# Optimization experiments

Measured on AMD Instinct MI355X. Metric: run time of the kernel, lower is better.

## Reference

```python
import jax, jax.numpy as jnp
import numpy as np

B, L, D = 32, 2048, 64
MASK_FILL = -1.0e6  # matches torch code's -1000000.0


def setup_inputs() -> dict:
    key = jax.random.key(0)
    kq, kk, kv, kl = jax.random.split(key, 4)
    queries = jax.random.normal(kq, (B, L, D), dtype=jnp.float32)
    keys = jax.random.normal(kk, (B, L, D), dtype=jnp.float32)
    values = jax.random.normal(kv, (B, L, D), dtype=jnp.float32)
    valid_lens = jax.random.randint(kl, (B,), 1, L + 1, dtype=jnp.int64)
    return {"queries": queries, "keys": keys, "values": values,
            "valid_lens": valid_lens}


def reference(queries, keys, values, valid_lens):
    d = queries.shape[-1]
    # [B, Lq, Lk] scores
    scores = jnp.einsum('bqd,bkd->bqk', queries, keys) / jnp.sqrt(
        jnp.asarray(d, dtype=queries.dtype))
    # length mask: position k valid iff k < valid_lens[b]
    Lk = scores.shape[-1]
    mask = jnp.arange(Lk)[None, :] < valid_lens[:, None]      # [B, Lk]
    scores = jnp.where(mask[:, None, :], scores, MASK_FILL)   # broadcast over Lq
    attn = jax.nn.softmax(scores, axis=-1)
    # dropout p=0.0 -> identity
    return jnp.einsum('bqk,bkv->bqv', attn, values)
```

## Files before the change

kernel.cpp:

```cpp
#include <hip/hip_runtime.h>
#include <hip/hip_bf16.h>
#include <math.h>


#define BB 32
#define LL 2048
#define DD 64
#define QBLK 128
#define KBLK 64
#define NTICKETS (BB * (LL / QBLK))
#define GRID 384

typedef __attribute__((ext_vector_type(8))) short bf16x8;
typedef __attribute__((ext_vector_type(4))) short bf16x4;
typedef __attribute__((ext_vector_type(4))) float f32x4;

static __device__ __forceinline__ short f2bf(float f) {
    __hip_bfloat16 h = __float2bfloat16(f);
    return *reinterpret_cast<short*>(&h);
}
static __device__ __forceinline__ unsigned pk2(float a, float b) {
    return (unsigned)(unsigned short)f2bf(a) | ((unsigned)(unsigned short)f2bf(b) << 16);
}
static __device__ __forceinline__ float exp2c(float x) {
    return __builtin_amdgcn_exp2f(x);
}

static __device__ __forceinline__ f32x4 mfma16(bf16x4 a, bf16x4 b, f32x4 c) {
#if __has_builtin(__builtin_amdgcn_mfma_f32_16x16x16bf16_1k)
    return __builtin_amdgcn_mfma_f32_16x16x16bf16_1k(a, b, c, 0, 0, 0);
#else
    asm("v_mfma_f32_16x16x16_bf16 %0, %1, %2, %0" : "+v"(c) : "v"(a), "v"(b));
    return c;
#endif
}

static __device__ __forceinline__ void cp16(const char* g, char* lbase, int lane) {
#if __has_builtin(__builtin_amdgcn_global_load_lds)
    __builtin_amdgcn_global_load_lds(
        (__attribute__((address_space(1))) void*)g,
        (__attribute__((address_space(3))) void*)lbase, 16, 0, 0);
#else
    *reinterpret_cast<uint4*>(lbase + lane * 16) = *reinterpret_cast<const uint4*>(g);
#endif
}

__global__ __launch_bounds__(256) void convert_kv_kernel(
    const float* __restrict__ K, const float* __restrict__ V,
    const int* __restrict__ vlen, unsigned short* __restrict__ kv,
    int* __restrict__ ws)
{
    const int tile = blockIdx.x;
    const int tid  = threadIdx.x;

    if (tile == 0) {
        if (tid == 32) ws[0] = 0;
        if (tid < BB) {
            int v = vlen[tid];
            int rank = 0;
            for (int j = 0; j < BB; ++j) {
                int vj = vlen[j];
                rank += (vj > v) || (vj == v && j < tid);
            }
            ws[1 + rank] = tid;
        }
    }

    const float*  Kt  = K + (size_t)tile * (KBLK * DD);
    const float4* Vg4 = reinterpret_cast<const float4*>(V + (size_t)tile * (KBLK * DD));
    unsigned short* img = kv + (size_t)tile * 8192;

    #pragma unroll
    for (int g = 0; g < 2; ++g) {
        int e = tid + g * 256;
        int f = e >> 6, L = e & 63;
        int t = f >> 1, ds = f & 1;
        int lq = L & 15, lg = L >> 4;
        const float4* src = reinterpret_cast<const float4*>(
            Kt + (t * 16 + lq) * DD + ds * 32 + lg * 8);
        float4 a = src[0], c = src[1];
        uint4 w;
        w.x = pk2(a.x, a.y); w.y = pk2(a.z, a.w);
        w.z = pk2(c.x, c.y); w.w = pk2(c.z, c.w);
        *reinterpret_cast<uint4*>(img + (size_t)e * 8) = w;
    }

    unsigned short* img2 = img + 4096;
    const int vd4 = (tid & 15) * 4;
    const int vkr = (tid >> 4) * 4;
    const int vt  = vkr >> 4;
    const int vlg = (vkr >> 2) & 3;
    float4 v0 = Vg4[(vkr + 0) * 16 + (tid & 15)];
    float4 v1 = Vg4[(vkr + 1) * 16 + (tid & 15)];
    float4 v2 = Vg4[(vkr + 2) * 16 + (tid & 15)];
    float4 v3 = Vg4[(vkr + 3) * 16 + (tid & 15)];
    const float* p0 = (const float*)&v0;
    const float* p1 = (const float*)&v1;
    const float* p2 = (const float*)&v2;
    const float* p3 = (const float*)&v3;
    #pragma unroll
    for (int j = 0; j < 4; ++j) {
        int col = vd4 + j;
        int n = col >> 4, lq = col & 15;
        int L = vlg * 16 + lq;
        uint2 w = make_uint2(pk2(p0[j], p1[j]), pk2(p2[j], p3[j]));
        *reinterpret_cast<uint2*>(img2 + (size_t)(n * 4 + vt) * 256 + L * 4) = w;
    }
}

__global__ __launch_bounds__(512, 1) void attn_mfma_kernel(
    const float* __restrict__ Q, const int* __restrict__ vlen,
    const unsigned short* __restrict__ kvimg,
    float* __restrict__ O, int* __restrict__ ws)
{
    __shared__ __align__(16) unsigned short Buf[3][8192];
    __shared__ int s_tile;

    int* ctr = ws;
    const int* order = ws + 1;

    const int tid  = threadIdx.x;
    const int wid  = tid >> 6;
    const int lane = tid & 63;
    const int lq   = lane & 15;
    const int lg   = lane >> 4;

    const float QSCALE = 0.125f * 1.44269504088896341f;

    for (;;) {
        __syncthreads();
        if (tid == 0) s_tile = atomicAdd(ctr, 1);
        __syncthreads();
        const int tile = s_tile;
        if (tile >= NTICKETS) break;

        const int b     = order[tile >> 4];
        const int qt    = tile & 15;
        const int qbase = qt * QBLK + wid * 16;
        const int valid = vlen[b];
        const int ntiles = (valid + KBLK - 1) / KBLK;

        const unsigned short* tbase = kvimg + (size_t)b * (32 * 8192);

        auto dma = [&](int t, int bi) {
            const char* g = (const char*)(tbase + (size_t)t * 8192)
                            + wid * 2048 + lane * 16;
            char* l = (char*)&Buf[bi][0] + wid * 2048;
            cp16(g,        l,        lane);
            cp16(g + 1024, l + 1024, lane);
        };

        bf16x8 qf[2];
        {
            const float* Qr = Q + ((size_t)b * LL + qbase + lq) * DD;
            #pragma unroll
            for (int ds_ = 0; ds_ < 2; ++ds_) {
                const float4* p4 = reinterpret_cast<const float4*>(Qr + ds_ * 32 + lg * 8);
                float4 a = p4[0], c = p4[1];
                bf16x8 f;
                f[0] = f2bf(a.x * QSCALE); f[1] = f2bf(a.y * QSCALE);
                f[2] = f2bf(a.z * QSCALE); f[3] = f2bf(a.w * QSCALE);
                f[4] = f2bf(c.x * QSCALE); f[5] = f2bf(c.y * QSCALE);
                f[6] = f2bf(c.z * QSCALE); f[7] = f2bf(c.w * QSCALE);
                qf[ds_] = f;
            }
        }

        f32x4 acc[4];
        #pragma unroll
        for (int n = 0; n < 4; ++n) acc[n] = (f32x4){0.f, 0.f, 0.f, 0.f};
        float m_ = -1e30f, l_ = 0.f;

        auto qkt = [&](int bi, f32x4* s) {
            const unsigned short* kb = &Buf[bi][0];
            __builtin_amdgcn_s_setprio(1);
            #pragma unroll
            for (int t = 0; t < 4; ++t) {
                f32x4 a = (f32x4){0.f, 0.f, 0.f, 0.f};
                #pragma unroll
                for (int ds_ = 0; ds_ < 2; ++ds_) {
                    bf16x8 kf = *reinterpret_cast<const bf16x8*>(
                        &kb[(size_t)(t * 2 + ds_) * 512 + lane * 8]);
                    a = __builtin_amdgcn_mfma_f32_16x16x32_bf16(kf, qf[ds_], a, 0, 0, 0);
                }
                s[t] = a;
            }
            __builtin_amdgcn_s_setprio(0);
        };

        auto smpv = [&](int kt, f32x4* s, int bi) {
            const bool tail = (kt == ntiles - 1) && (valid & (KBLK - 1));
            if (tail) {
                #pragma unroll
                for (int t = 0; t < 4; ++t)
                    #pragma unroll
                    for (int r = 0; r < 4; ++r) {
                        int kg = kt * KBLK + t * 16 + lg * 4 + r;
                        if (kg >= valid) s[t][r] = -1e30f;
                    }
            }
            float mx = s[0][0];
            #pragma unroll
            for (int t = 0; t < 4; ++t)
                #pragma unroll
                for (int r = 0; r < 4; ++r) mx = fmaxf(mx, s[t][r]);
            mx = fmaxf(mx, __shfl_xor(mx, 16, 64));
            mx = fmaxf(mx, __shfl_xor(mx, 32, 64));

            if (__any(mx - m_ > 8.0f)) {
                float mnew = fmaxf(m_, mx);
                float corr = exp2c(m_ - mnew);
                m_ = mnew;
                l_ *= corr;
                #pragma unroll
                for (int r = 0; r < 4; ++r) {
                    float cq = __shfl(corr, lg * 4 + r, 64);
                    #pragma unroll
                    for (int n = 0; n < 4; ++n) acc[n][r] *= cq;
                }
            }

            float ls = 0.f;
            #pragma unroll
            for (int t = 0; t < 4; ++t)
                #pragma unroll
                for (int r = 0; r < 4; ++r) {
                    float p = exp2c(s[t][r] - m_);
                    s[t][r] = p;
                    ls += p;
                }
            ls += __shfl_xor(ls, 16, 64);
            ls += __shfl_xor(ls, 32, 64);
            l_ += ls;

            const unsigned short* vb = &Buf[bi][4096];
            __builtin_amdgcn_s_setprio(1);
            #pragma unroll
            for (int t = 0; t < 4; ++t) {
                union { uint2 u; bf16x4 v; } pa;
                pa.u = make_uint2(pk2(s[t][0], s[t][1]), pk2(s[t][2], s[t][3]));
                #pragma unroll
                for (int n = 0; n < 4; ++n) {
                    union { uint2 u; bf16x4 v; } vv;
                    vv.u = *reinterpret_cast<const uint2*>(
                        &vb[(size_t)(n * 4 + t) * 256 + lane * 4]);
                    acc[n] = mfma16(pa.v, vv.v, acc[n]);
                }
            }
            __builtin_amdgcn_s_setprio(0);
        };

        int bc = 0, bn = 1, bd = 2;
        dma(0, 0);
        if (ntiles > 1) dma(1, 1);
        __syncthreads();
        f32x4 sA[4], sB[4];
        qkt(0, sA);

        int t = 0;
        for (; t + 2 <= ntiles; t += 2) {
            if (t + 2 < ntiles) dma(t + 2, bd);
            qkt(bn, sB);
            smpv(t, sA, bc);
            __syncthreads();
            { int x = bc; bc = bn; bn = bd; bd = x; }
            if (t + 3 < ntiles) dma(t + 3, bd);
            if (t + 2 < ntiles) qkt(bn, sA);
            smpv(t + 1, sB, bc);
            __syncthreads();
            { int x = bc; bc = bn; bn = bd; bd = x; }
        }
        if (t < ntiles) smpv(t, sA, bc);

        float linv[4];
        #pragma unroll
        for (int r = 0; r < 4; ++r)
            linv[r] = 1.f / __shfl(l_, lg * 4 + r, 64);
        float* Ob = O + ((size_t)b * LL + qbase) * DD;
        #pragma unroll
        for (int n = 0; n < 4; ++n) {
            #pragma unroll
            for (int r = 0; r < 4; ++r) {
                Ob[(size_t)(lg * 4 + r) * DD + n * 16 + lq] = acc[n][r] * linv[r];
            }
        }
    }
}

extern "C" void kernel_launch(void* const* d_in, const int* in_sizes, int n_in,
                              void* d_out, int out_size, void* d_ws, size_t ws_size,
                              hipStream_t stream) {
    const float* Q = (const float*)d_in[0];
    const float* K = (const float*)d_in[1];
    const float* V = (const float*)d_in[2];
    const int* vlen = (const int*)d_in[3];
    float* O = (float*)d_out;

    int* ws_i = (int*)d_ws;
    unsigned short* kvimg = (unsigned short*)((char*)d_ws + 1024);

    convert_kv_kernel<<<BB * (LL / KBLK), 256, 0, stream>>>(K, V, vlen, kvimg, ws_i);
    attn_mfma_kernel<<<GRID, 512, 0, stream>>>(Q, vlen, kvimg, O, ws_i);
}
```

Before: 64.44 us.

## Process key tiles in pairs with dual softmax states and four-buffer ring

Restructures the main loop to load two K/V tiles per iteration into a four-slot LDS ring, compute both QK^T products, then run two independent online-softmax streams (separate max, sum and accumulators) that are merged at the end. This halves the number of block barriers per tile and interleaves two independent dependency chains to raise ILP around the exp/reduction and MFMA work. In exchange it doubles accumulator registers, uses more LDS (64KB), and loses the previous overlap of the next tile's QK^T with the current softmax.

```diff
diff --git a/kernel.cpp b/kernel.cpp
--- a/kernel.cpp
+++ b/kernel.cpp
@@ -113,7 +113,7 @@
     const unsigned short* __restrict__ kvimg,
     float* __restrict__ O, int* __restrict__ ws)
 {
-    __shared__ __align__(16) unsigned short Buf[3][8192];
+    __shared__ __align__(16) unsigned short Buf[4][8192];
     __shared__ int s_tile;
 
     int* ctr = ws;
@@ -142,10 +142,13 @@
 
         const unsigned short* tbase = kvimg + (size_t)b * (32 * 8192);
 
-        auto dma = [&](int t, int bi) {
+        auto bufp = [&](int t) -> const unsigned short* {
+            return (const unsigned short*)((const char*)&Buf[0][0] + ((t & 3) << 14));
+        };
+        auto dma = [&](int t) {
             const char* g = (const char*)(tbase + (size_t)t * 8192)
                             + wid * 2048 + lane * 16;
-            char* l = (char*)&Buf[bi][0] + wid * 2048;
+            char* l = (char*)&Buf[0][0] + ((t & 3) << 14) + wid * 2048;
             cp16(g,        l,        lane);
             cp16(g + 1024, l + 1024, lane);
         };
@@ -166,13 +169,16 @@
             }
         }
 
-        f32x4 acc[4];
+        f32x4 accA[4], accB[4];
         #pragma unroll
-        for (int n = 0; n < 4; ++n) acc[n] = (f32x4){0.f, 0.f, 0.f, 0.f};
-        float m_ = -1e30f, l_ = 0.f;
-
-        auto qkt = [&](int bi, f32x4* s) {
-            const unsigned short* kb = &Buf[bi][0];
+        for (int n = 0; n < 4; ++n) {
+            accA[n] = (f32x4){0.f, 0.f, 0.f, 0.f};
+            accB[n] = (f32x4){0.f, 0.f, 0.f, 0.f};
+        }
+        float mA_ = -1e30f, lA_ = 0.f;
+        float mB_ = -1e30f, lB_ = 0.f;
+
+        auto qkt = [&](const unsigned short* kb, f32x4* s) {
             __builtin_amdgcn_s_setprio(1);
             #pragma unroll
             for (int t = 0; t < 4; ++t) {
@@ -188,7 +194,91 @@
             __builtin_amdgcn_s_setprio(0);
         };
 
-        auto smpv = [&](int kt, f32x4* s, int bi) {
+        auto smpv2 = [&](int ktA, f32x4* sa, f32x4* sb,
+                         const unsigned short* vbA, const unsigned short* vbB) {
+            const bool tailB = (ktA + 2 == ntiles) && (valid & (KBLK - 1));
+            if (tailB) {
+                #pragma unroll
+                for (int t = 0; t < 4; ++t)
+                    #pragma unroll
+                    for (int r = 0; r < 4; ++r) {
+                        int kg = (ktA + 1) * KBLK + t * 16 + lg * 4 + r;
+                        if (kg >= valid) sb[t][r] = -1e30f;
+                    }
+            }
+            float pA[4], pB[4];
+            #pragma unroll
+            for (int t = 0; t < 4; ++t) {
+                pA[t] = fmaxf(fmaxf(sa[t][0], sa[t][1]), fmaxf(sa[t][2], sa[t][3]));
+                pB[t] = fmaxf(fmaxf(sb[t][0], sb[t][1]), fmaxf(sb[t][2], sb[t][3]));
+            }
+            float mxA = fmaxf(fmaxf(pA[0], pA[1]), fmaxf(pA[2], pA[3]));
+            float mxB = fmaxf(fmaxf(pB[0], pB[1]), fmaxf(pB[2], pB[3]));
+            mxA = fmaxf(mxA, __shfl_xor(mxA, 16, 64));
+            mxB = fmaxf(mxB, __shfl_xor(mxB, 16, 64));
+            mxA = fmaxf(mxA, __shfl_xor(mxA, 32, 64));
+            mxB = fmaxf(mxB, __shfl_xor(mxB, 32, 64));
+
+            float grow = fmaxf(mxA - mA_, mxB - mB_);
+            if (__any(grow > 8.0f)) {
+                float mnA = fmaxf(mA_, mxA), mnB = fmaxf(mB_, mxB);
+                float cA = exp2c(mA_ - mnA), cB = exp2c(mB_ - mnB);
+                mA_ = mnA; mB_ = mnB;
+                lA_ *= cA;  lB_ *= cB;
+                #pragma unroll
+                for (int r = 0; r < 4; ++r) {
+                    float cqA = __shfl(cA, lg * 4 + r, 64);
+                    float cqB = __shfl(cB, lg * 4 + r, 64);
+                    #pragma unroll
+                    for (int n = 0; n < 4; ++n) {
+                        accA[n][r] *= cqA;
+                        accB[n][r] *= cqB;
+                    }
+                }
+            }
+
+            #pragma unroll
+            for (int t = 0; t < 4; ++t)
+                #pragma unroll
+                for (int r = 0; r < 4; ++r) {
+                    sa[t][r] = exp2c(sa[t][r] - mA_);
+                    sb[t][r] = exp2c(sb[t][r] - mB_);
+                }
+            #pragma unroll
+            for (int t = 0; t < 4; ++t) {
+                pA[t] = (sa[t][0] + sa[t][1]) + (sa[t][2] + sa[t][3]);
+                pB[t] = (sb[t][0] + sb[t][1]) + (sb[t][2] + sb[t][3]);
+            }
+            float lsA = (pA[0] + pA[1]) + (pA[2] + pA[3]);
+            float lsB = (pB[0] + pB[1]) + (pB[2] + pB[3]);
+            lsA += __shfl_xor(lsA, 16, 64);
+            lsB += __shfl_xor(lsB, 16, 64);
+            lsA += __shfl_xor(lsA, 32, 64);
+            lsB += __shfl_xor(lsB, 32, 64);
+            lA_ += lsA;
+            lB_ += lsB;
+
+            __builtin_amdgcn_s_setprio(1);
+            #pragma unroll
+            for (int t = 0; t < 4; ++t) {
+                union { uint2 u; bf16x4 v; } paA, paB;
+                paA.u = make_uint2(pk2(sa[t][0], sa[t][1]), pk2(sa[t][2], sa[t][3]));
+                paB.u = make_uint2(pk2(sb[t][0], sb[t][1]), pk2(sb[t][2], sb[t][3]));
+                #pragma unroll
+                for (int n = 0; n < 4; ++n) {
+                    union { uint2 u; bf16x4 v; } vA, vB;
+                    vA.u = *reinterpret_cast<const uint2*>(
+                        &vbA[(size_t)(n * 4 + t) * 256 + lane * 4]);
+                    vB.u = *reinterpret_cast<const uint2*>(
+                        &vbB[(size_t)(n * 4 + t) * 256 + lane * 4]);
+                    accA[n] = mfma16(paA.v, vA.v, accA[n]);
+                    accB[n] = mfma16(paB.v, vB.v, accB[n]);
+                }
+            }
+            __builtin_amdgcn_s_setprio(0);
+        };
+
+        auto smpv1 = [&](int kt, f32x4* s, const unsigned short* vb) {
             const bool tail = (kt == ntiles - 1) && (valid & (KBLK - 1));
             if (tail) {
                 #pragma unroll
@@ -199,41 +289,39 @@
                         if (kg >= valid) s[t][r] = -1e30f;
                     }
             }
-            float mx = s[0][0];
+            float pA[4];
             #pragma unroll
             for (int t = 0; t < 4; ++t)
-                #pragma unroll
-                for (int r = 0; r < 4; ++r) mx = fmaxf(mx, s[t][r]);
+                pA[t] = fmaxf(fmaxf(s[t][0], s[t][1]), fmaxf(s[t][2], s[t][3]));
+            float mx = fmaxf(fmaxf(pA[0], pA[1]), fmaxf(pA[2], pA[3]));
             mx = fmaxf(mx, __shfl_xor(mx, 16, 64));
             mx = fmaxf(mx, __shfl_xor(mx, 32, 64));
 
-            if (__any(mx - m_ > 8.0f)) {
-                float mnew = fmaxf(m_, mx);
-                float corr = exp2c(m_ - mnew);
-                m_ = mnew;
-                l_ *= corr;
+            if (__any(mx - mA_ > 8.0f)) {
+                float mnew = fmaxf(mA_, mx);
+                float corr = exp2c(mA_ - mnew);
+                mA_ = mnew;
+                lA_ *= corr;
                 #pragma unroll
                 for (int r = 0; r < 4; ++r) {
                     float cq = __shfl(corr, lg * 4 + r, 64);
                     #pragma unroll
-                    for (int n = 0; n < 4; ++n) acc[n][r] *= cq;
-                }
-            }
-
-            float ls = 0.f;
+                    for (int n = 0; n < 4; ++n) accA[n][r] *= cq;
+                }
+            }
             #pragma unroll
             for (int t = 0; t < 4; ++t)
                 #pragma unroll
-                for (int r = 0; r < 4; ++r) {
-                    float p = exp2c(s[t][r] - m_);
-                    s[t][r] = p;
-                    ls += p;
-                }
+                for (int r = 0; r < 4; ++r)
+                    s[t][r] = exp2c(s[t][r] - mA_);
+            #pragma unroll
+            for (int t = 0; t < 4; ++t)
+                pA[t] = (s[t][0] + s[t][1]) + (s[t][2] + s[t][3]);
+            float ls = (pA[0] + pA[1]) + (pA[2] + pA[3]);
             ls += __shfl_xor(ls, 16, 64);
             ls += __shfl_xor(ls, 32, 64);
-            l_ += ls;
-
-            const unsigned short* vb = &Buf[bi][4096];
+            lA_ += ls;
+
             __builtin_amdgcn_s_setprio(1);
             #pragma unroll
             for (int t = 0; t < 4; ++t) {
@@ -244,44 +332,45 @@
                     union { uint2 u; bf16x4 v; } vv;
                     vv.u = *reinterpret_cast<const uint2*>(
                         &vb[(size_t)(n * 4 + t) * 256 + lane * 4]);
-                    acc[n] = mfma16(pa.v, vv.v, acc[n]);
+                    accA[n] = mfma16(pa.v, vv.v, accA[n]);
                 }
             }
             __builtin_amdgcn_s_setprio(0);
         };
 
-        int bc = 0, bn = 1, bd = 2;
-        dma(0, 0);
-        if (ntiles > 1) dma(1, 1);
+        dma(0);
+        if (ntiles > 1) dma(1);
         __syncthreads();
+
         f32x4 sA[4], sB[4];
-        qkt(0, sA);
-
         int t = 0;
         for (; t + 2 <= ntiles; t += 2) {
-            if (t + 2 < ntiles) dma(t + 2, bd);
-            qkt(bn, sB);
-            smpv(t, sA, bc);
+            if (t + 2 < ntiles) dma(t + 2);
+            if (t + 3 < ntiles) dma(t + 3);
+            qkt(bufp(t),     sA);
+            qkt(bufp(t + 1), sB);
+            smpv2(t, sA, sB, bufp(t) + 4096, bufp(t + 1) + 4096);
             __syncthreads();
-            { int x = bc; bc = bn; bn = bd; bd = x; }
-            if (t + 3 < ntiles) dma(t + 3, bd);
-            if (t + 2 < ntiles) qkt(bn, sA);
-            smpv(t + 1, sB, bc);
-            __syncthreads();
-            { int x = bc; bc = bn; bn = bd; bd = x; }
-        }
-        if (t < ntiles) smpv(t, sA, bc);
-
-        float linv[4];
-        #pragma unroll
-        for (int r = 0; r < 4; ++r)
-            linv[r] = 1.f / __shfl(l_, lg * 4 + r, 64);
+        }
+        if (t < ntiles) {
+            qkt(bufp(t), sA);
+            smpv1(t, sA, bufp(t) + 4096);
+        }
+
+        float M   = fmaxf(mA_, mB_);
+        float wA  = exp2c(mA_ - M);
+        float wB  = exp2c(mB_ - M);
+        float inv = 1.f / (wA * lA_ + wB * lB_);
+        float fA = wA * inv, fB = wB * inv;
         float* Ob = O + ((size_t)b * LL + qbase) * DD;
         #pragma unroll
-        for (int n = 0; n < 4; ++n) {
-            #pragma unroll
-            for (int r = 0; r < 4; ++r) {
-                Ob[(size_t)(lg * 4 + r) * DD + n * 16 + lq] = acc[n][r] * linv[r];
+        for (int r = 0; r < 4; ++r) {
+            float gA = __shfl(fA, lg * 4 + r, 64);
+            float gB = __shfl(fB, lg * 4 + r, 64);
+            #pragma unroll
+            for (int n = 0; n < 4; ++n) {
+                Ob[(size_t)(lg * 4 + r) * DD + n * 16 + lq] =
+                    accA[n][r] * gA + accB[n][r] * gB;
             }
         }
     }
```

New measurement: 63.55 us. About the same (-1.4%).
